# Kernel optimization log

Measured on AMD Instinct MI355X. Metric: run time of the kernel, lower is better.

The kernel has to match this reference:

```python
import jax, jax.numpy as jnp
import numpy as np

FLT_BACKWARP = 2.5  # Matching.fltBackwarp for intLevel == 4
NEG_SLOPE = 0.1


def backwarp(ten_input, ten_flow):
    # torch grid_sample(mode='bilinear', padding_mode='zeros', align_corners=True)
    # with grid = base + flow*2/(size-1) is equivalent to sampling at pixel coords
    # (x + u, y + v) with zero padding outside [0, W-1] x [0, H-1].
    B, C, H, W = ten_input.shape
    xs = jnp.arange(W, dtype=ten_input.dtype)
    ys = jnp.arange(H, dtype=ten_input.dtype)
    px = xs[None, None, :] + ten_flow[:, 0]  # [B,H,W]
    py = ys[None, :, None] + ten_flow[:, 1]  # [B,H,W]
    x0 = jnp.floor(px)
    y0 = jnp.floor(py)
    x1 = x0 + 1.0
    y1 = y0 + 1.0
    wx1 = px - x0
    wx0 = 1.0 - wx1
    wy1 = py - y0
    wy0 = 1.0 - wy1

    def gather(ix, iy):
        valid = ((ix >= 0) & (ix <= W - 1) & (iy >= 0) & (iy <= H - 1)).astype(ten_input.dtype)
        ixc = jnp.clip(ix, 0, W - 1).astype(jnp.int32)
        iyc = jnp.clip(iy, 0, H - 1).astype(jnp.int32)
        v = jax.vmap(lambda img, yy, xx: img[:, yy, xx])(ten_input, iyc, ixc)  # [B,C,H,W]
        return v * valid[:, None]

    return (gather(x0, y0) * (wx0 * wy0)[:, None]
            + gather(x1, y0) * (wx1 * wy0)[:, None]
            + gather(x0, y1) * (wx0 * wy1)[:, None]
            + gather(x1, y1) * (wx1 * wy1)[:, None])


def correlation(one, two, stride):
    # FunctionCorrelation: 7x7 displacement window, offsets (-3..3)*stride,
    # zero pad 3*stride, dot over channels / C. Output [B,49,ceil(H/s),ceil(W/s)].
    B, C, H, W = one.shape
    p = 3 * stride
    two_pad = jnp.pad(two, ((0, 0), (0, 0), (p, p), (p, p)))
    one_s = one[:, :, ::stride, ::stride]  # [B,C,Ho,Wo]
    outs = []
    for dj in range(-3, 4):  # channel index k = (dj+3)*7 + (di+3)
        for di in range(-3, 4):
            y0 = p + dj * stride
            x0 = p + di * stride
            shift = two_pad[:, :, y0:y0 + H:stride, x0:x0 + W:stride]
            outs.append(jnp.einsum('bchw,bchw->bhw', one_s, shift))
    return jnp.stack(outs, axis=1) / jnp.asarray(C, one.dtype)


def setup_inputs() -> dict:
    key = jax.random.key(0)
    k1, k2, k3 = jax.random.split(key, 3)
    B, C, H, W = 2, 128, 256, 448
    return {
        'tenOne': jax.random.normal(k1, (B, C, H, W), dtype=jnp.float32),
        'tenTwo': jax.random.normal(k2, (B, C, H, W), dtype=jnp.float32),
        'tenFlow': jax.random.normal(k3, (B, 2, H, W), dtype=jnp.float32),
        'intStride': 1,
    }


def reference(tenOne, tenTwo, tenFlow, intStride):
    warped = backwarp(tenTwo, tenFlow * FLT_BACKWARP)
    corr = correlation(tenOne, warped, int(intStride))
    return jax.nn.leaky_relu(corr, NEG_SLOPE)
```

## Files before the change

### kernel.cpp

```cpp
#include <hip/hip_runtime.h>
#include <hip/hip_bf16.h>

#define BB 2
#define CC 128
#define HH 256
#define WW 448
#define KK 49
#define HWSZ (HH * WW)
#define PW 456

#define WT_BYTES ((size_t)BB * HH * PW * CC * 2)
#define TWT_BYTES ((size_t)BB * HH * WW * CC * 2)
#define WS_NEED (WT_BYTES + TWT_BYTES)

typedef __attribute__((ext_vector_type(8))) short bf16x8;
typedef __attribute__((ext_vector_type(4))) float f32x4;
typedef __attribute__((ext_vector_type(8))) unsigned short u16x8;

static __device__ __forceinline__ short f2bf(float v) {
  __hip_bfloat16 h = __float2bfloat16(v);
  return *reinterpret_cast<short*>(&h);
}
static __device__ __forceinline__ float bf2f(unsigned short u) {
  unsigned int x = ((unsigned int)u) << 16;
  return __uint_as_float(x);
}

typedef const __attribute__((address_space(1))) unsigned int* as1_u32p;
typedef __attribute__((address_space(3))) unsigned int* as3_u32p;
static __device__ __forceinline__ void gload_lds16(const void* g, void* l) {
  __builtin_amdgcn_global_load_lds((as1_u32p)g, (as3_u32p)l, 16, 0, 0);
}

__global__ __launch_bounds__(256) void border_kernel(__hip_bfloat16* wt) {
  int i = blockIdx.x * 256 + threadIdx.x;
  int by = i >> 7;
  int r = i & 127;
  int ps = r >> 4;
  int c16 = r & 15;
  int px = (ps < 4) ? ps : (448 + ps);
  u16x8 z = {0, 0, 0, 0, 0, 0, 0, 0};
  *(u16x8*)((char*)wt + ((size_t)((size_t)by * PW + px) * CC + c16 * 8) * 2) = z;
}

__global__ __launch_bounds__(256) void transpose_kernel(
    const float* __restrict__ two, __hip_bfloat16* __restrict__ two_t,
    __hip_bfloat16* __restrict__ wt) {
  __shared__ float lds[128 * 33];
  int bid = blockIdx.x;
  if (bid < 256) {
    int i = bid * 256 + threadIdx.x;
    int by = i >> 7;
    int r = i & 127;
    int ps = r >> 4;
    int c16 = r & 15;
    int px = (ps < 4) ? ps : (448 + ps);
    u16x8 z = {0, 0, 0, 0, 0, 0, 0, 0};
    *(u16x8*)((char*)wt + ((size_t)((size_t)by * PW + px) * CC + c16 * 8) * 2) =
        z;
  }
  int b = bid / (HWSZ / 32);
  int tile = bid - b * (HWSZ / 32);
  int P0 = tile * 32;

  const float* src = two + (size_t)b * CC * HWSZ + P0;
  int t = threadIdx.x;
  int bc = t >> 3;
  int f = t & 7;
#pragma unroll
  for (int k = 0; k < 4; ++k) {
    int c = bc + k * 32;
    float4 v = *(const float4*)(src + (size_t)c * HWSZ + f * 4);
    float* d = &lds[c * 33 + f * 4];
    d[0] = v.x; d[1] = v.y; d[2] = v.z; d[3] = v.w;
  }
  __syncthreads();

  int q = t & 7;
  int pl = t >> 3;
  int cs = q * 16;
  u16x8 pk0, pk1;
#pragma unroll
  for (int j = 0; j < 8; ++j)
    pk0[j] = (unsigned short)f2bf(lds[(cs + j) * 33 + pl]);
#pragma unroll
  for (int j = 0; j < 8; ++j)
    pk1[j] = (unsigned short)f2bf(lds[(cs + 8 + j) * 33 + pl]);
  char* dst = (char*)two_t + ((size_t)((size_t)b * HWSZ + P0 + pl) * CC + cs) * 2;
  *(u16x8*)dst = pk0;
  *(u16x8*)(dst + 16) = pk1;
}

__global__ __launch_bounds__(1024) void warp_fast(
    const __hip_bfloat16* __restrict__ two_t, const float* __restrict__ flow,
    __hip_bfloat16* __restrict__ wt) {
  int bid = blockIdx.x;
  int wg = (bid & 7) * 448 + (bid >> 3);
  int b = wg / 1792;
  int rem = wg - b * 1792;
  int y = rem / 7;
  int seg = rem - y * 7;
  int pg = threadIdx.x >> 4;
  int cw = threadIdx.x & 15;
  int x = seg * 64 + pg;

  float fx = flow[(size_t)(b * 2 + 0) * HWSZ + y * WW + x] * 2.5f;
  float fy = flow[(size_t)(b * 2 + 1) * HWSZ + y * WW + x] * 2.5f;
  float px = (float)x + fx;
  float py = (float)y + fy;
  float x0f = floorf(px), y0f = floorf(py);
  int x0 = (int)x0f, y0 = (int)y0f;
  int x1 = x0 + 1, y1 = y0 + 1;
  float wx1 = px - x0f, wx0 = 1.0f - wx1;
  float wy1 = py - y0f, wy0 = 1.0f - wy1;
  bool vx0 = (x0 >= 0) && (x0 < WW);
  bool vx1 = (x1 >= 0) && (x1 < WW);
  bool vy0 = (y0 >= 0) && (y0 < HH);
  bool vy1 = (y1 >= 0) && (y1 < HH);
  float w00 = (vx0 && vy0) ? wx0 * wy0 : 0.0f;
  float w01 = (vx1 && vy0) ? wx1 * wy0 : 0.0f;
  float w10 = (vx0 && vy1) ? wx0 * wy1 : 0.0f;
  float w11 = (vx1 && vy1) ? wx1 * wy1 : 0.0f;
  int cx0 = min(max(x0, 0), WW - 1);
  int cx1 = min(max(x1, 0), WW - 1);
  int cy0 = min(max(y0, 0), HH - 1);
  int cy1 = min(max(y1, 0), HH - 1);

  const char* tb = (const char*)two_t + (size_t)b * HWSZ * (CC * 2);
  u16x8 a = *(const u16x8*)(tb + ((size_t)cy0 * WW + cx0) * 256 + cw * 16);
  u16x8 bb_ = *(const u16x8*)(tb + ((size_t)cy0 * WW + cx1) * 256 + cw * 16);
  u16x8 c = *(const u16x8*)(tb + ((size_t)cy1 * WW + cx0) * 256 + cw * 16);
  u16x8 d = *(const u16x8*)(tb + ((size_t)cy1 * WW + cx1) * 256 + cw * 16);

  u16x8 pk;
#pragma unroll
  for (int e = 0; e < 8; ++e) {
    float v = w00 * bf2f((unsigned short)a[e]) +
              w01 * bf2f((unsigned short)bb_[e]) +
              w10 * bf2f((unsigned short)c[e]) +
              w11 * bf2f((unsigned short)d[e]);
    pk[e] = (unsigned short)f2bf(v);
  }
  *(u16x8*)((char*)wt + ((size_t)(b * HH + y) * PW + x + 4) * (CC * 2) +
            cw * 16) = pk;
}

__global__ __launch_bounds__(256) void warp_fallback(
    const float* __restrict__ two, const float* __restrict__ flow,
    __hip_bfloat16* __restrict__ wt) {
  int idx = blockIdx.x * 256 + threadIdx.x;
  if (idx >= BB * HWSZ) return;
  int x = idx % WW;
  int y = (idx / WW) % HH;
  int b = idx / HWSZ;

  float fx = flow[(b * 2 + 0) * HWSZ + y * WW + x] * 2.5f;
  float fy = flow[(b * 2 + 1) * HWSZ + y * WW + x] * 2.5f;
  float px = (float)x + fx;
  float py = (float)y + fy;
  float x0f = floorf(px), y0f = floorf(py);
  int x0 = (int)x0f, y0 = (int)y0f;
  int x1 = x0 + 1, y1 = y0 + 1;
  float wx1 = px - x0f, wx0 = 1.0f - wx1;
  float wy1 = py - y0f, wy0 = 1.0f - wy1;
  bool vx0 = (x0 >= 0) && (x0 < WW);
  bool vx1 = (x1 >= 0) && (x1 < WW);
  bool vy0 = (y0 >= 0) && (y0 < HH);
  bool vy1 = (y1 >= 0) && (y1 < HH);
  float w00 = (vx0 && vy0) ? wx0 * wy0 : 0.0f;
  float w01 = (vx1 && vy0) ? wx1 * wy0 : 0.0f;
  float w10 = (vx0 && vy1) ? wx0 * wy1 : 0.0f;
  float w11 = (vx1 && vy1) ? wx1 * wy1 : 0.0f;
  int cx0 = min(max(x0, 0), WW - 1);
  int cx1 = min(max(x1, 0), WW - 1);
  int cy0 = min(max(y0, 0), HH - 1);
  int cy1 = min(max(y1, 0), HH - 1);
  int o00 = cy0 * WW + cx0;
  int o01 = cy0 * WW + cx1;
  int o10 = cy1 * WW + cx0;
  int o11 = cy1 * WW + cx1;

  const float* p = two + (size_t)b * CC * HWSZ;
  char* wo = (char*)wt + ((size_t)((size_t)(b * HH + y) * PW) + x + 4) * CC * 2;
#pragma unroll 4
  for (int j = 0; j < 16; ++j) {
    u16x8 pk;
#pragma unroll
    for (int jj = 0; jj < 8; ++jj) {
      int c = j * 8 + jj;
      const float* pc = p + (size_t)c * HWSZ;
      float v = w00 * pc[o00] + w01 * pc[o01] + w10 * pc[o10] + w11 * pc[o11];
      pk[jj] = (unsigned short)f2bf(v);
    }
    *(u16x8*)(wo + j * 16) = pk;
  }
}

#define YTB 8
#define NROWS 14
#define NPOS 22
#define ROWCH (NPOS * 16)
#define CHUNKS (NROWS * ROWCH)

__global__ __launch_bounds__(512, 4) void corr_kernel(
    const float* __restrict__ one, const __hip_bfloat16* __restrict__ wt,
    float* __restrict__ out) {
  __shared__ uint4 ldsb[CHUNKS];

  int bid = blockIdx.x;
  int wg = (bid & 7) * 224 + (bid >> 3);
  int b = wg / 896;
  int rem = wg - b * 896;
  int xt = rem >> 5;
  int yt = rem & 31;
  int ybase = yt * YTB;
  int X0 = xt * 16;
  int tid = threadIdx.x;
  int w = tid >> 6;
  int l = tid & 63;
  int lp = l & 15;
  int lg = l >> 4;
  int y = ybase + w;

  const char* wbase =
      (const char*)wt + (((size_t)(b * HH)) * PW + X0 + 1) * (CC * 2);
  bool interior = (ybase >= 3) && (ybase + NROWS - 3 <= HH);

  if (interior) {
#pragma unroll
    for (int k = 0; k < 10; ++k) {
      int ci = tid + k * 512;
      if (k < 9 || tid < (CHUNKS - 9 * 512)) {
        int row = ci / ROWCH;
        int r2 = ci - row * ROWCH;
        int p = r2 >> 4;
        int cw = r2 & 15;
        int cwS = cw ^ (p & 15);
        int yy = ybase - 3 + row;
        const char* g = wbase + (size_t)yy * (PW * CC * 2) + p * 256 + cwS * 16;
        int wave_ci0 = k * 512 + (tid & ~63);
        gload_lds16(g, (char*)ldsb + (size_t)wave_ci0 * 16);
      }
    }
  } else {
#pragma unroll
    for (int k = 0; k < 10; ++k) {
      int ci = tid + k * 512;
      if (ci < CHUNKS) {
        int row = ci / ROWCH;
        int r2 = ci - row * ROWCH;
        int p = r2 >> 4;
        int cw = r2 & 15;
        int yy = ybase - 3 + row;
        uint4 v = {0, 0, 0, 0};
        if (yy >= 0 && yy < HH)
          v = *(const uint4*)(wbase + (size_t)yy * (PW * CC * 2) + p * 256 +
                              cw * 16);
        *(uint4*)((char*)ldsb + ((ci * 16) ^ ((p & 15) << 4))) = v;
      }
    }
  }

  const float* Abase = one + ((size_t)(b * CC) * HH + y) * WW + X0 + lp;
  bf16x8 afr[4];
#pragma unroll
  for (int t = 0; t < 4; ++t)
#pragma unroll
    for (int j = 0; j < 8; ++j)
      afr[t][j] = f2bf(Abase[(size_t)(t * 32 + lg * 8 + j) * HWSZ]);

  __syncthreads();

  int p1 = (lp + 16 < 21) ? (lp + 16) : 21;
  int cosw0[4], cosw1[4];
#pragma unroll
  for (int t = 0; t < 4; ++t) {
    int co = t * 64 + lg * 16;
    cosw0[t] = co ^ ((lp & 15) << 4);
    cosw1[t] = co ^ ((p1 & 15) << 4);
  }

  f32x4 acc[7][2] = {};
#pragma unroll
  for (int dj = 0; dj < 7; ++dj) {
    int rl = w + dj;
    int b0 = (rl * NPOS + lp) << 8;
    int b1 = (rl * NPOS + p1) << 8;
#pragma unroll
    for (int t = 0; t < 4; ++t) {
      bf16x8 v0 = *(const bf16x8*)((const char*)ldsb + (b0 + cosw0[t]));
      bf16x8 v1 = *(const bf16x8*)((const char*)ldsb + (b1 + cosw1[t]));
      acc[dj][0] = __builtin_amdgcn_mfma_f32_16x16x32_bf16(afr[t], v0,
                                                           acc[dj][0], 0, 0, 0);
      acc[dj][1] = __builtin_amdgcn_mfma_f32_16x16x32_bf16(afr[t], v1,
                                                           acc[dj][1], 0, 0, 0);
    }
  }

  __syncthreads();
  float* sc = (float*)ldsb;
#pragma unroll
  for (int dj = 0; dj < 7; ++dj) {
#pragma unroll
    for (int nt = 0; nt < 2; ++nt) {
      int post = lp + 16 * nt;
#pragma unroll
      for (int r = 0; r < 4; ++r) {
        int xlc = 4 * lg + r;
        int di = post - xlc;
        if (di >= 0 && di <= 6) {
          int k = dj * 7 + di;
          sc[k * 128 + w * 16 + ((xlc + k) & 15)] = acc[dj][nt][r];
        }
      }
    }
  }
  __syncthreads();

  float* ob = out + (size_t)(b * KK) * HWSZ + (size_t)ybase * WW + X0;
#pragma unroll
  for (int i = 0; i < 13; ++i) {
    int e = tid + i * 512;
    if (e < KK * 128) {
      int k = e >> 7;
      int yr = (e >> 4) & 7;
      int px = e & 15;
      float v = sc[k * 128 + yr * 16 + ((px + k) & 15)] * (1.0f / 128.0f);
      v = (v > 0.0f) ? v : 0.1f * v;
      ob[(size_t)k * HWSZ + yr * WW + px] = v;
    }
  }
}

extern "C" void kernel_launch(void* const* d_in, const int* in_sizes, int n_in,
                              void* d_out, int out_size, void* d_ws,
                              size_t ws_size, hipStream_t stream) {
  const float* tenOne = (const float*)d_in[0];
  const float* tenTwo = (const float*)d_in[1];
  const float* tenFlow = (const float*)d_in[2];

  __hip_bfloat16* wt = (__hip_bfloat16*)d_ws;

  if (ws_size >= WS_NEED) {
    __hip_bfloat16* two_t = (__hip_bfloat16*)((char*)d_ws + WT_BYTES);
    transpose_kernel<<<BB * (HWSZ / 32), 256, 0, stream>>>(tenTwo, two_t, wt);
    warp_fast<<<3584, 1024, 0, stream>>>(two_t, tenFlow, wt);
  } else {
    border_kernel<<<256, 256, 0, stream>>>(wt);
    int blocks = (BB * HWSZ + 255) / 256;
    warp_fallback<<<blocks, 256, 0, stream>>>(tenTwo, tenFlow, wt);
  }
  corr_kernel<<<1792, 512, 0, stream>>>(tenOne, wt, (float*)d_out);
}
```

Measured before the change: 130.1 us.

## Stage warped tile in two channel halves to halve LDS footprint

The correlation kernel now loads the warped bf16 tile into shared memory in two 64-channel halves, using a half-sized LDS buffer. Each half gets its own swizzle, and its MFMA pass reads the matching A fragments. Halving the LDS allocation is meant to let more workgroups fit on each CU, so that memory latency in one block hides behind compute in others. The cost is extra barriers and a serialized load-compute-load-compute sequence inside each block, with no double buffering.

```diff
diff --git a/kernel.cpp b/kernel.cpp
--- a/kernel.cpp
+++ b/kernel.cpp
@@ -199,13 +199,13 @@
 #define YTB 8
 #define NROWS 14
 #define NPOS 22
-#define ROWCH (NPOS * 16)
-#define CHUNKS (NROWS * ROWCH)
+#define HROWCH (NPOS * 8)
+#define HCHUNKS (NROWS * HROWCH)
 
 __global__ __launch_bounds__(512, 4) void corr_kernel(
     const float* __restrict__ one, const __hip_bfloat16* __restrict__ wt,
     float* __restrict__ out) {
-  __shared__ uint4 ldsb[CHUNKS];
+  __shared__ uint4 ldsb[HCHUNKS];
 
   int bid = blockIdx.x;
   int wg = (bid & 7) * 224 + (bid >> 3);
@@ -226,41 +226,40 @@
       (const char*)wt + (((size_t)(b * HH)) * PW + X0 + 1) * (CC * 2);
   bool interior = (ybase >= 3) && (ybase + NROWS - 3 <= HH);
 
-  if (interior) {
-#pragma unroll
-    for (int k = 0; k < 10; ++k) {
-      int ci = tid + k * 512;
-      if (k < 9 || tid < (CHUNKS - 9 * 512)) {
-        int row = ci / ROWCH;
-        int r2 = ci - row * ROWCH;
-        int p = r2 >> 4;
-        int cw = r2 & 15;
-        int cwS = cw ^ (p & 15);
-        int yy = ybase - 3 + row;
-        const char* g = wbase + (size_t)yy * (PW * CC * 2) + p * 256 + cwS * 16;
-        int wave_ci0 = k * 512 + (tid & ~63);
-        gload_lds16(g, (char*)ldsb + (size_t)wave_ci0 * 16);
-      }
-    }
-  } else {
-#pragma unroll
-    for (int k = 0; k < 10; ++k) {
-      int ci = tid + k * 512;
-      if (ci < CHUNKS) {
-        int row = ci / ROWCH;
-        int r2 = ci - row * ROWCH;
-        int p = r2 >> 4;
-        int cw = r2 & 15;
-        int yy = ybase - 3 + row;
-        uint4 v = {0, 0, 0, 0};
-        if (yy >= 0 && yy < HH)
-          v = *(const uint4*)(wbase + (size_t)yy * (PW * CC * 2) + p * 256 +
-                              cw * 16);
-        *(uint4*)((char*)ldsb + ((ci * 16) ^ ((p & 15) << 4))) = v;
-      }
-    }
-  }
-
+#define STAGE_HALF(H)                                                         \
+  if (interior) {                                                             \
+    _Pragma("unroll") for (int k = 0; k < 5; ++k) {                           \
+      int ci = tid + k * 512;                                                 \
+      if (ci < HCHUNKS) {                                                     \
+        int row = ci / HROWCH;                                                \
+        int r2 = ci - row * HROWCH;                                           \
+        int p = r2 >> 3;                                                      \
+        int cw = r2 & 7;                                                      \
+        int yy = ybase - 3 + row;                                             \
+        const char* g = wbase + (size_t)yy * (PW * CC * 2) + p * 256 +        \
+                        (H)*128 + (cw ^ (p & 7)) * 16;                        \
+        gload_lds16(g, (char*)ldsb + (size_t)(k * 512 + (tid & ~63)) * 16);   \
+      }                                                                       \
+    }                                                                         \
+  } else {                                                                    \
+    _Pragma("unroll") for (int k = 0; k < 5; ++k) {                           \
+      int ci = tid + k * 512;                                                 \
+      if (ci < HCHUNKS) {                                                     \
+        int row = ci / HROWCH;                                                \
+        int r2 = ci - row * HROWCH;                                           \
+        int p = r2 >> 3;                                                      \
+        int cw = r2 & 7;                                                      \
+        int yy = ybase - 3 + row;                                             \
+        uint4 v = {0, 0, 0, 0};                                               \
+        if (yy >= 0 && yy < HH)                                               \
+          v = *(const uint4*)(wbase + (size_t)yy * (PW * CC * 2) + p * 256 +  \
+                              (H)*128 + cw * 16);                             \
+        *(uint4*)((char*)ldsb + ((ci * 16) ^ ((p & 7) << 4))) = v;            \
+      }                                                                       \
+    }                                                                         \
+  }
+
+  STAGE_HALF(0)
   const float* Abase = one + ((size_t)(b * CC) * HH + y) * WW + X0 + lp;
   bf16x8 afr[4];
 #pragma unroll
@@ -269,30 +268,50 @@
     for (int j = 0; j < 8; ++j)
       afr[t][j] = f2bf(Abase[(size_t)(t * 32 + lg * 8 + j) * HWSZ]);
 
-  __syncthreads();
-
   int p1 = (lp + 16 < 21) ? (lp + 16) : 21;
-  int cosw0[4], cosw1[4];
-#pragma unroll
-  for (int t = 0; t < 4; ++t) {
-    int co = t * 64 + lg * 16;
-    cosw0[t] = co ^ ((lp & 15) << 4);
-    cosw1[t] = co ^ ((p1 & 15) << 4);
+  int cs0[2], cs1[2];
+#pragma unroll
+  for (int tl = 0; tl < 2; ++tl) {
+    cs0[tl] = ((tl * 4 + lg) ^ (lp & 7)) << 4;
+    cs1[tl] = ((tl * 4 + lg) ^ (p1 & 7)) << 4;
   }
 
   f32x4 acc[7][2] = {};
+
+  __syncthreads();
+
 #pragma unroll
   for (int dj = 0; dj < 7; ++dj) {
     int rl = w + dj;
-    int b0 = (rl * NPOS + lp) << 8;
-    int b1 = (rl * NPOS + p1) << 8;
-#pragma unroll
-    for (int t = 0; t < 4; ++t) {
-      bf16x8 v0 = *(const bf16x8*)((const char*)ldsb + (b0 + cosw0[t]));
-      bf16x8 v1 = *(const bf16x8*)((const char*)ldsb + (b1 + cosw1[t]));
-      acc[dj][0] = __builtin_amdgcn_mfma_f32_16x16x32_bf16(afr[t], v0,
+    int b0 = (rl * NPOS + lp) << 7;
+    int b1 = (rl * NPOS + p1) << 7;
+#pragma unroll
+    for (int tl = 0; tl < 2; ++tl) {
+      bf16x8 v0 = *(const bf16x8*)((const char*)ldsb + (b0 + cs0[tl]));
+      bf16x8 v1 = *(const bf16x8*)((const char*)ldsb + (b1 + cs1[tl]));
+      acc[dj][0] = __builtin_amdgcn_mfma_f32_16x16x32_bf16(afr[tl], v0,
                                                            acc[dj][0], 0, 0, 0);
-      acc[dj][1] = __builtin_amdgcn_mfma_f32_16x16x32_bf16(afr[t], v1,
+      acc[dj][1] = __builtin_amdgcn_mfma_f32_16x16x32_bf16(afr[tl], v1,
+                                                           acc[dj][1], 0, 0, 0);
+    }
+  }
+
+  __syncthreads();
+  STAGE_HALF(1)
+  __syncthreads();
+
+#pragma unroll
+  for (int dj = 0; dj < 7; ++dj) {
+    int rl = w + dj;
+    int b0 = (rl * NPOS + lp) << 7;
+    int b1 = (rl * NPOS + p1) << 7;
+#pragma unroll
+    for (int tl = 0; tl < 2; ++tl) {
+      bf16x8 v0 = *(const bf16x8*)((const char*)ldsb + (b0 + cs0[tl]));
+      bf16x8 v1 = *(const bf16x8*)((const char*)ldsb + (b1 + cs1[tl]));
+      acc[dj][0] = __builtin_amdgcn_mfma_f32_16x16x32_bf16(afr[2 + tl], v0,
+                                                           acc[dj][0], 0, 0, 0);
+      acc[dj][1] = __builtin_amdgcn_mfma_f32_16x16x32_bf16(afr[2 + tl], v1,
                                                            acc[dj][1], 0, 0, 0);
     }
   }
@@ -330,6 +349,7 @@
       ob[(size_t)k * HWSZ + yr * WW + px] = v;
     }
   }
+#undef STAGE_HALF
 }
 
 extern "C" void kernel_launch(void* const* d_in, const int* in_sizes, int n_in,
```

Measured after the change: 132.8 us. 2.1% more time.

## Split LDS staging into two channel halves to overlap loads with MFMA

Applied to the files above, without the earlier changes.

The correlation kernel now stages the warped tile into two LDS buffers, one per 64-channel half, instead of one buffer holding all channels. In the interior path it issues the first half's global-to-LDS loads, then the A-fragment loads, then the second half's loads, and starts MFMA work on the first half before waiting on the second. The goal is to hide part of the global load latency behind compute. The cost is extra barriers, scheduling fences and more index arithmetic. Correctness leans on in-order vmcnt behaviour, and the score scratch stores land only in buffer 0, which every wave has finished reading once the second barrier is passed.

```diff
diff --git a/kernel.cpp b/kernel.cpp
--- a/kernel.cpp
+++ b/kernel.cpp
@@ -199,13 +199,14 @@
 #define YTB 8
 #define NROWS 14
 #define NPOS 22
-#define ROWCH (NPOS * 16)
-#define CHUNKS (NROWS * ROWCH)
+#define HROWCH (NPOS * 8)
+#define HCHUNKS (NROWS * HROWCH)
+#define HBYTES (HCHUNKS * 16)
 
 __global__ __launch_bounds__(512, 4) void corr_kernel(
     const float* __restrict__ one, const __hip_bfloat16* __restrict__ wt,
     float* __restrict__ out) {
-  __shared__ uint4 ldsb[CHUNKS];
+  __shared__ uint4 ldsb[2][HCHUNKS];
 
   int bid = blockIdx.x;
   int wg = (bid & 7) * 224 + (bid >> 3);
@@ -226,78 +227,104 @@
       (const char*)wt + (((size_t)(b * HH)) * PW + X0 + 1) * (CC * 2);
   bool interior = (ybase >= 3) && (ybase + NROWS - 3 <= HH);
 
-  if (interior) {
-#pragma unroll
-    for (int k = 0; k < 10; ++k) {
-      int ci = tid + k * 512;
-      if (k < 9 || tid < (CHUNKS - 9 * 512)) {
-        int row = ci / ROWCH;
-        int r2 = ci - row * ROWCH;
-        int p = r2 >> 4;
-        int cw = r2 & 15;
-        int cwS = cw ^ (p & 15);
-        int yy = ybase - 3 + row;
-        const char* g = wbase + (size_t)yy * (PW * CC * 2) + p * 256 + cwS * 16;
-        int wave_ci0 = k * 512 + (tid & ~63);
-        gload_lds16(g, (char*)ldsb + (size_t)wave_ci0 * 16);
-      }
-    }
-  } else {
-#pragma unroll
-    for (int k = 0; k < 10; ++k) {
-      int ci = tid + k * 512;
-      if (ci < CHUNKS) {
-        int row = ci / ROWCH;
-        int r2 = ci - row * ROWCH;
-        int p = r2 >> 4;
-        int cw = r2 & 15;
-        int yy = ybase - 3 + row;
-        uint4 v = {0, 0, 0, 0};
-        if (yy >= 0 && yy < HH)
-          v = *(const uint4*)(wbase + (size_t)yy * (PW * CC * 2) + p * 256 +
-                              cw * 16);
-        *(uint4*)((char*)ldsb + ((ci * 16) ^ ((p & 15) << 4))) = v;
-      }
-    }
+#define STAGE_HALF_G(H, BUF)                                                  \
+  _Pragma("unroll") for (int k = 0; k < 5; ++k) {                             \
+    int ci = tid + k * 512;                                                   \
+    if (ci < HCHUNKS) {                                                       \
+      int row = ci / HROWCH;                                                  \
+      int r2 = ci - row * HROWCH;                                             \
+      int p = r2 >> 3;                                                        \
+      int cw = r2 & 7;                                                        \
+      int yy = ybase - 3 + row;                                               \
+      const char* g = wbase + (size_t)yy * (PW * CC * 2) + p * 256 +          \
+                      (H)*128 + (cw ^ (p & 7)) * 16;                          \
+      gload_lds16(g, (char*)ldsb + (BUF)*HBYTES +                             \
+                         (size_t)(k * 512 + (tid & ~63)) * 16);               \
+    }                                                                         \
+  }
+
+#define STAGE_HALF_E(H, BUF)                                                  \
+  _Pragma("unroll") for (int k = 0; k < 5; ++k) {                             \
+    int ci = tid + k * 512;                                                   \
+    if (ci < HCHUNKS) {                                                       \
+      int row = ci / HROWCH;                                                  \
+      int r2 = ci - row * HROWCH;                                             \
+      int p = r2 >> 3;                                                        \
+      int cw = r2 & 7;                                                        \
+      int yy = ybase - 3 + row;                                               \
+      uint4 v = {0, 0, 0, 0};                                                 \
+      if (yy >= 0 && yy < HH)                                                 \
+        v = *(const uint4*)(wbase + (size_t)yy * (PW * CC * 2) + p * 256 +    \
+                            (H)*128 + cw * 16);                               \
+      *(uint4*)((char*)ldsb + (BUF)*HBYTES + ((ci * 16) ^ ((p & 7) << 4))) =  \
+          v;                                                                  \
+    }                                                                         \
+  }
+
+#define COMPUTE_HALF(BUF, T0)                                                 \
+  _Pragma("unroll") for (int dj = 0; dj < 7; ++dj) {                          \
+    int rl = w + dj;                                                          \
+    int b0 = (rl * NPOS + lp) << 7;                                           \
+    int b1 = (rl * NPOS + p1) << 7;                                           \
+    _Pragma("unroll") for (int tl = 0; tl < 2; ++tl) {                        \
+      bf16x8 v0 = *(const bf16x8*)((const char*)ldsb + (BUF)*HBYTES +         \
+                                   (b0 + cs0[tl]));                           \
+      bf16x8 v1 = *(const bf16x8*)((const char*)ldsb + (BUF)*HBYTES +         \
+                                   (b1 + cs1[tl]));                           \
+      acc[dj][0] = __builtin_amdgcn_mfma_f32_16x16x32_bf16(                   \
+          afr[(T0) + tl], v0, acc[dj][0], 0, 0, 0);                           \
+      acc[dj][1] = __builtin_amdgcn_mfma_f32_16x16x32_bf16(                   \
+          afr[(T0) + tl], v1, acc[dj][1], 0, 0, 0);                           \
+    }                                                                         \
   }
 
   const float* Abase = one + ((size_t)(b * CC) * HH + y) * WW + X0 + lp;
   bf16x8 afr[4];
-#pragma unroll
-  for (int t = 0; t < 4; ++t)
-#pragma unroll
-    for (int j = 0; j < 8; ++j)
-      afr[t][j] = f2bf(Abase[(size_t)(t * 32 + lg * 8 + j) * HWSZ]);
-
-  __syncthreads();
-
   int p1 = (lp + 16 < 21) ? (lp + 16) : 21;
-  int cosw0[4], cosw1[4];
-#pragma unroll
-  for (int t = 0; t < 4; ++t) {
-    int co = t * 64 + lg * 16;
-    cosw0[t] = co ^ ((lp & 15) << 4);
-    cosw1[t] = co ^ ((p1 & 15) << 4);
-  }
-
+  int cs0[2], cs1[2];
+#pragma unroll
+  for (int tl = 0; tl < 2; ++tl) {
+    cs0[tl] = ((tl * 4 + lg) ^ (lp & 7)) << 4;
+    cs1[tl] = ((tl * 4 + lg) ^ (p1 & 7)) << 4;
+  }
   f32x4 acc[7][2] = {};
-#pragma unroll
-  for (int dj = 0; dj < 7; ++dj) {
-    int rl = w + dj;
-    int b0 = (rl * NPOS + lp) << 8;
-    int b1 = (rl * NPOS + p1) << 8;
-#pragma unroll
-    for (int t = 0; t < 4; ++t) {
-      bf16x8 v0 = *(const bf16x8*)((const char*)ldsb + (b0 + cosw0[t]));
-      bf16x8 v1 = *(const bf16x8*)((const char*)ldsb + (b1 + cosw1[t]));
-      acc[dj][0] = __builtin_amdgcn_mfma_f32_16x16x32_bf16(afr[t], v0,
-                                                           acc[dj][0], 0, 0, 0);
-      acc[dj][1] = __builtin_amdgcn_mfma_f32_16x16x32_bf16(afr[t], v1,
-                                                           acc[dj][1], 0, 0, 0);
-    }
-  }
-
-  __syncthreads();
+
+  if (interior) {
+    STAGE_HALF_G(0, 0)
+    __builtin_amdgcn_sched_barrier(0);
+#pragma unroll
+    for (int t = 0; t < 4; ++t)
+#pragma unroll
+      for (int j = 0; j < 8; ++j)
+        afr[t][j] = f2bf(Abase[(size_t)(t * 32 + lg * 8 + j) * HWSZ]);
+    __builtin_amdgcn_sched_barrier(0);
+    STAGE_HALF_G(1, 1)
+    __builtin_amdgcn_sched_barrier(0);
+    __builtin_amdgcn_s_barrier();
+    __builtin_amdgcn_sched_barrier(0);
+
+    COMPUTE_HALF(0, 0)
+
+    asm volatile("s_waitcnt vmcnt(0)" ::: "memory");
+    __builtin_amdgcn_sched_barrier(0);
+    __builtin_amdgcn_s_barrier();
+    __builtin_amdgcn_sched_barrier(0);
+
+    COMPUTE_HALF(1, 2)
+  } else {
+    STAGE_HALF_E(0, 0)
+    STAGE_HALF_E(1, 1)
+#pragma unroll
+    for (int t = 0; t < 4; ++t)
+#pragma unroll
+      for (int j = 0; j < 8; ++j)
+        afr[t][j] = f2bf(Abase[(size_t)(t * 32 + lg * 8 + j) * HWSZ]);
+    __syncthreads();
+    COMPUTE_HALF(0, 0)
+    COMPUTE_HALF(1, 2)
+    __syncthreads();
+  }
+
   float* sc = (float*)ldsb;
 #pragma unroll
   for (int dj = 0; dj < 7; ++dj) {
@@ -330,6 +357,9 @@
       ob[(size_t)k * HWSZ + yr * WW + px] = v;
     }
   }
+#undef STAGE_HALF_G
+#undef STAGE_HALF_E
+#undef COMPUTE_HALF
 }
 
 extern "C" void kernel_launch(void* const* d_in, const int* in_sizes, int n_in,
```

Result: no change. 131.2 us (+0.8%).
